# Performance work log

Hardware: AMD Instinct MI355X
Metric: run time of the kernel (lower is better)

## Reference

```python
import jax, jax.numpy as jnp
from jax import lax
import numpy as np

NB_CODE = 16384
DIM = 128
SCALES = [(1, 1), (2, 2), (4, 4), (8, 8), (16, 16)]
PHI_IDX = [0, 1, 1, 2, 3]  # PhiPartiallyShared: argmin(|ticks - si/(SN-1)|), K=4, SN=5
RESI = 0.5  # abs(quant_resi)
BETA = 0.25


def _cubic(x, a=-0.75):
    # PyTorch bicubic kernel (cubic convolution, a=-0.75)
    ax = np.abs(x)
    return np.where(ax <= 1.0, (a + 2.0) * ax ** 3 - (a + 3.0) * ax ** 2 + 1.0,
                    np.where(ax < 2.0, a * ax ** 3 - 5.0 * a * ax ** 2 + 8.0 * a * ax - 4.0 * a, 0.0))


def bicubic_mat(n_in, n_out):
    # 1D interpolation matrix matching torch F.interpolate(mode='bicubic', align_corners=False)
    W = np.zeros((n_out, n_in), dtype=np.float32)
    scale = n_in / n_out
    for i in range(n_out):
        x = (i + 0.5) * scale - 0.5
        x0 = int(np.floor(x))
        t = x - x0
        for k in range(4):
            idx = min(max(x0 - 1 + k, 0), n_in - 1)  # border clamp
            W[i, idx] += _cubic(t + 1.0 - k)
    return jnp.asarray(W)


def phi_apply(h, w, b):
    y = lax.conv_general_dilated(h, w, (1, 1), 'SAME',
                                 dimension_numbers=('NCHW', 'OIHW', 'NCHW'))
    y = y + b[None, :, None, None]
    return h * (1.0 - RESI) + y * RESI


def setup_inputs() -> dict:
    key = jax.random.key(0)
    k1, k2, k3, k4 = jax.random.split(key, 4)
    B, C, J, L = 16, DIM, 16, 16
    f_bcjl = jax.random.normal(k1, (B, C, J, L), dtype=jnp.float32)
    emb = jax.random.normal(k2, (NB_CODE, C), dtype=jnp.float32) * 0.02
    # 4 partially-shared Phi convs (3x3, C->C)
    phi_w = jax.random.normal(k3, (4, C, C, 3, 3), dtype=jnp.float32) * (1.0 / np.sqrt(C * 9))
    phi_b = jax.random.normal(k4, (4, C), dtype=jnp.float32) * 0.01
    return {'f_bcjl': f_bcjl, 'emb': emb, 'phi_w': phi_w, 'phi_b': phi_b}


def reference(f_bcjl, emb, phi_w, phi_b):
    B, C, J, L = f_bcjl.shape
    SN = len(SCALES)
    f_ng = lax.stop_gradient(f_bcjl)
    f_rest = f_ng
    f_hat = jnp.zeros_like(f_ng)
    loss = jnp.float32(0.0)
    e_sq = jnp.sum(emb * emb, axis=1)  # [K]
    idx_all = []
    for si, (sn, tn) in enumerate(SCALES):
        if si != SN - 1:
            # 'area' downsample == integer-factor average pooling here
            r = f_rest.reshape(B, C, sn, J // sn, tn, L // tn).mean(axis=(3, 5))
        else:
            r = f_rest
        rNC = r.transpose(0, 2, 3, 1).reshape(-1, C)  # [N, C]
        d = jnp.sum(rNC * rNC, axis=1, keepdims=True) + e_sq - 2.0 * (rNC @ emb.T)
        idx = jnp.argmin(d, axis=1)  # [N]
        idx_all.append(idx)
        h = emb[idx].reshape(B, sn, tn, C).transpose(0, 3, 1, 2)  # [B,C,sn,tn]
        if si != SN - 1:
            Wj = bicubic_mat(sn, J)
            Wl = bicubic_mat(tn, L)
            h = jnp.einsum('js,bcst,lt->bcjl', Wj, h, Wl)
        k = PHI_IDX[si]
        h = phi_apply(h, phi_w[k], phi_b[k])
        f_hat = f_hat + h
        f_rest = f_rest - h
        loss = loss + BETA * jnp.mean((lax.stop_gradient(f_hat) - f_bcjl) ** 2) \
                    + jnp.mean((f_hat - f_ng) ** 2)
    loss = loss / SN
    idx_cat = jnp.concatenate(idx_all)
    counts = jnp.zeros((NB_CODE,), jnp.float32).at[idx_cat].add(1.0)
    p = counts / idx_cat.shape[0]
    perplexity = jnp.exp(-jnp.sum(p * jnp.log(p + 1e-10)))
    # straight-through estimator
    f_hat_out = lax.stop_gradient(f_hat) - f_ng + f_bcjl
    return (f_hat_out, loss, perplexity)
```

## Files before the change

kernel.cpp:

```cpp
#include <hip/hip_runtime.h>
#include <hip/hip_bf16.h>
#include <math.h>

#define BATCH 16
#define CDIM  128
#define NCODE 16384
#define ELEMS 524288
#define NTOT  5456
#define WEXT_TOT 589824
#define LOSS_COEF 4.76837158203125e-7f

typedef __attribute__((ext_vector_type(8))) short short8;
typedef __attribute__((ext_vector_type(4))) float float4v;
typedef unsigned short ushortT;
typedef unsigned long long u64;
typedef unsigned int u32;

__device__ __forceinline__ ushortT f2bf(float x) {
    __hip_bfloat16 h = __float2bfloat16(x);
    return *reinterpret_cast<ushortT*>(&h);
}
__device__ __forceinline__ float bf2f(ushortT b) {
    __hip_bfloat16 h = *reinterpret_cast<__hip_bfloat16*>(&b);
    return __bfloat162float(h);
}
__device__ __forceinline__ u32 ford(float v) {
    u32 b = __float_as_uint(v);
    return b ^ ((u32)((int)b >> 31) | 0x80000000u);
}

__device__ double cubic_d(double x) {
    const double a = -0.75;
    double ax = fabs(x);
    if (ax <= 1.0) return (a + 2.0) * ax * ax * ax - (a + 3.0) * ax * ax + 1.0;
    if (ax < 2.0)  return a * ax * ax * ax - 5.0 * a * ax * ax + 8.0 * a * ax - 4.0 * a;
    return 0.0;
}

__global__ __launch_bounds__(256)
void k_prologue(const float* __restrict__ f, const float* __restrict__ emb,
                const float* __restrict__ phi_w,
                float* __restrict__ f_rest, float* __restrict__ f_hat,
                float* __restrict__ esq, ushortT* __restrict__ embext,
                ushortT* __restrict__ wext, float* __restrict__ wmat,
                float* __restrict__ lossA) {
    const int t = threadIdx.x;
    const int id = blockIdx.x * 256 + t;

    if (id < ELEMS) {
        f_rest[id] = f[id];
        f_hat[id] = 0.f;
        int row = id >> 5, c4 = id & 31;
        float4 v = reinterpret_cast<const float4*>(emb + (size_t)row * CDIM)[c4];
        float xs[4] = {v.x, v.y, v.z, v.w};
        ushortT hi[4], lo[4];
        float ss = 0.f;
        #pragma unroll
        for (int i = 0; i < 4; ++i) {
            hi[i] = f2bf(xs[i]);
            lo[i] = f2bf(xs[i] - bf2f(hi[i]));
            ss += xs[i] * xs[i];
        }
        ushortT* base = embext + (size_t)row * 256;
        *reinterpret_cast<ushort4*>(base + c4 * 4)       = make_ushort4(hi[0], hi[1], hi[2], hi[3]);
        *reinterpret_cast<ushort4*>(base + 128 + c4 * 4) = make_ushort4(lo[0], lo[1], lo[2], lo[3]);
        #pragma unroll
        for (int off = 16; off; off >>= 1) ss += __shfl_down(ss, off);
        if ((t & 31) == 0) esq[row] = ss;
    }
    if (id < WEXT_TOT) {
        int k4 = id / 147456, rem = id % 147456;
        int co = rem / 1152, kk = rem % 1152;
        int off = kk >> 7, ci = kk & 127;
        float v = 0.5f * phi_w[(((size_t)(k4 * 128 + co)) * 128 + ci) * 9 + off];
        if (ci == co && off == 4) v += 0.5f;
        wext[id] = f2bf(v);
    }
    if (blockIdx.x == 0 && t < 64) {
        int sIdx = t >> 4;
        int S = 1 << sIdx;
        int j = t & 15;
        const int offs[4] = {0, 16, 48, 112};
        double row[8];
        for (int s = 0; s < 8; ++s) row[s] = 0.0;
        double scale = (double)S / 16.0;
        double x = (j + 0.5) * scale - 0.5;
        double x0 = floor(x);
        double tt = x - x0;
        for (int k = 0; k < 4; ++k) {
            int idx = (int)x0 - 1 + k;
            idx = idx < 0 ? 0 : (idx > S - 1 ? S - 1 : idx);
            row[idx] += cubic_d(tt + 1.0 - k);
        }
        for (int s = 0; s < S; ++s) wmat[offs[sIdx] + j * S + s] = (float)row[s];
    }
    if (id == 0) lossA[0] = 0.f;
}

__global__ __launch_bounds__(256)
void k_packext(const float* __restrict__ fr, ushortT* __restrict__ re,
               u64* __restrict__ packed, int N, int padN, int S, int lgS) {
    int id = blockIdx.x * 256 + threadIdx.x;
    if (id < N) packed[id] = ~0ull;
    if (id >= padN * 32) return;
    int row = id >> 5, c4 = id & 31;
    ushortT hi[4], lo[4];
    if (row < N) {
        int mask = S - 1;
        int tt = row & mask, ssi = (row >> lgS) & mask, b = row >> (2 * lgS);
        int bs = 16 >> lgS;
        float inv = 1.f / (float)(bs * bs);
        #pragma unroll
        for (int u = 0; u < 4; ++u) {
            int c = c4 * 4 + u;
            const float* base = fr + (size_t)(b * 128 + c) * 256 + (ssi * bs) * 16 + tt * bs;
            float acc = 0.f;
            for (int jj = 0; jj < bs; ++jj)
                for (int ll = 0; ll < bs; ++ll)
                    acc += base[jj * 16 + ll];
            float x = acc * inv;
            hi[u] = f2bf(x);
            lo[u] = f2bf(x - bf2f(hi[u]));
        }
    } else {
        #pragma unroll
        for (int u = 0; u < 4; ++u) { hi[u] = 0; lo[u] = 0; }
    }
    ushortT* base = re + (size_t)row * 256;
    *reinterpret_cast<ushort4*>(base + c4 * 4)       = make_ushort4(hi[0], hi[1], hi[2], hi[3]);
    *reinterpret_cast<ushort4*>(base + 128 + c4 * 4) = make_ushort4(lo[0], lo[1], lo[2], lo[3]);
}

__global__ __launch_bounds__(256)
void k_packext_wave(const float* __restrict__ fr, ushortT* __restrict__ re,
                    u64* __restrict__ packed, int N, int padN, int S, int lgS) {
    int gid = blockIdx.x * 256 + threadIdx.x;
    int wid = gid >> 6, lane = threadIdx.x & 63;
    if (wid >= padN * 128) return;
    int row = wid >> 7, c = wid & 127;
    float x = 0.f;
    if (row < N) {
        int mask = S - 1;
        int tt = row & mask, ssi = (row >> lgS) & mask, b = row >> (2 * lgS);
        int lgbs = 4 - lgS, bs = 1 << lgbs, cnt = bs * bs;
        const float* base = fr + (size_t)(b * 128 + c) * 256 + (ssi * bs) * 16 + tt * bs;
        float acc = 0.f;
        for (int e = lane; e < cnt; e += 64)
            acc += base[(e >> lgbs) * 16 + (e & (bs - 1))];
        #pragma unroll
        for (int off = 32; off; off >>= 1) acc += __shfl_down(acc, off);
        x = acc / (float)cnt;
    }
    if (lane == 0) {
        ushortT h = f2bf(x);
        re[(size_t)row * 256 + c] = h;
        re[(size_t)row * 256 + 128 + c] = f2bf(x - bf2f(h));
        if (c == 0 && row < N) packed[row] = ~0ull;
    }
}

__global__ __launch_bounds__(256)
void k_argmin_mfma(const ushortT* __restrict__ rext, const ushortT* __restrict__ embext,
                   const float* __restrict__ esq, int N, int kPerSplit,
                   u64* __restrict__ packed) {
    __shared__ ushortT Btile[2][64 * 32 * 8];
    const int t = threadIdx.x;
    const int w = t >> 6;
    const int lane = t & 63;
    const int ln = lane & 15;
    const int q  = lane >> 4;
    const int k0beg = blockIdx.y * kPerSplit;
    const int rowW = blockIdx.x * 128 + w * 32;

    short8 a[2][8];
    {
        const ushortT* r0 = rext + (size_t)(rowW + ln) * 256 + q * 8;
        const ushortT* r1 = rext + (size_t)(rowW + 16 + ln) * 256 + q * 8;
        #pragma unroll
        for (int sb = 0; sb < 8; ++sb) {
            a[0][sb] = *reinterpret_cast<const short8*>(r0 + sb * 32);
            a[1][sb] = *reinterpret_cast<const short8*>(r1 + sb * 32);
        }
    }

    float minv[2][4];
    int   mini[2][4];
    #pragma unroll
    for (int tt = 0; tt < 2; ++tt)
        #pragma unroll
        for (int rg = 0; rg < 4; ++rg) { minv[tt][rg] = 3.4e38f; mini[tt][rg] = 0; }

    const int tiles = kPerSplit >> 6;

    #pragma unroll
    for (int i = 0; i < 8; ++i) {
        int F = (i * 4 + w) * 64 + lane;
        int n = F >> 5, cs = F & 31;
        int cp = (cs & ~7) | ((cs & 7) ^ (n & 7));
        const ushortT* src = embext + (size_t)(k0beg + n) * 256 + cp * 8;
        __builtin_amdgcn_global_load_lds(
            (const __attribute__((address_space(1))) unsigned int*)src,
            (__attribute__((address_space(3))) unsigned int*)&Btile[0][(size_t)((i * 4 + w) * 64) * 8],
            16, 0, 0);
    }

    for (int it = 0; it < tiles; ++it) {
        __syncthreads();
        if (it + 1 < tiles) {
            int k1 = k0beg + (it + 1) * 64;
            int bu = (it + 1) & 1;
            #pragma unroll
            for (int i = 0; i < 8; ++i) {
                int F = (i * 4 + w) * 64 + lane;
                int n = F >> 5, cs = F & 31;
                int cp = (cs & ~7) | ((cs & 7) ^ (n & 7));
                const ushortT* src = embext + (size_t)(k1 + n) * 256 + cp * 8;
                __builtin_amdgcn_global_load_lds(
                    (const __attribute__((address_space(1))) unsigned int*)src,
                    (__attribute__((address_space(3))) unsigned int*)&Btile[bu][(size_t)((i * 4 + w) * 64) * 8],
                    16, 0, 0);
            }
        }
        const ushortT* Bt = Btile[it & 1];
        const int k0 = k0beg + it * 64;

        #pragma unroll
        for (int sub = 0; sub < 4; ++sub) {
            int n = sub * 16 + ln;
            short8 bfr[8];
            #pragma unroll
            for (int sb = 0; sb < 8; ++sb) {
                int cp = q + 4 * sb;
                int cs = (cp & ~7) | ((cp & 7) ^ (n & 7));
                bfr[sb] = *reinterpret_cast<const short8*>(&Bt[(size_t)(n * 32 + cs) * 8]);
            }
            float4v acc0 = {0.f, 0.f, 0.f, 0.f};
            float4v acc1 = {0.f, 0.f, 0.f, 0.f};
            #pragma unroll
            for (int s = 0; s < 12; ++s) {
                int as = s < 8 ? s : s - 8;
                int bs = s < 4 ? s : s - 4;
                acc0 = __builtin_amdgcn_mfma_f32_16x16x32_bf16(a[0][as], bfr[bs], acc0, 0, 0, 0);
                acc1 = __builtin_amdgcn_mfma_f32_16x16x32_bf16(a[1][as], bfr[bs], acc1, 0, 0, 0);
            }
            int kc = k0 + sub * 16 + ln;
            float es = esq[kc];
            #pragma unroll
            for (int rg = 0; rg < 4; ++rg) {
                float sc0 = fmaf(-2.f, acc0[rg], es);
                if (sc0 < minv[0][rg]) { minv[0][rg] = sc0; mini[0][rg] = kc; }
                float sc1 = fmaf(-2.f, acc1[rg], es);
                if (sc1 < minv[1][rg]) { minv[1][rg] = sc1; mini[1][rg] = kc; }
            }
        }
    }

    #pragma unroll
    for (int tt = 0; tt < 2; ++tt)
        #pragma unroll
        for (int rg = 0; rg < 4; ++rg) {
            float v = minv[tt][rg]; int ix = mini[tt][rg];
            #pragma unroll
            for (int off = 1; off < 16; off <<= 1) {
                float ov = __shfl_xor(v, off);
                int   oi = __shfl_xor(ix, off);
                if (ov < v || (ov == v && oi < ix)) { v = ov; ix = oi; }
            }
            if (ln == 0) {
                int row = rowW + tt * 16 + q * 4 + rg;
                if (row < N) {
                    u64 p = ((u64)ford(v) << 32) | (u32)ix;
                    atomicMin(&packed[row], p);
                }
            }
        }
}

__global__ __launch_bounds__(256)
void k_upconv(const float* __restrict__ emb, const u64* __restrict__ packed,
              const float* __restrict__ wm, int S, int lastScale,
              const ushortT* __restrict__ wext, const float* __restrict__ bias,
              const float* __restrict__ f_in, float* __restrict__ f_hat,
              float* __restrict__ f_rest, float* __restrict__ loss_acc) {
    __shared__ __align__(16) ushortT Htile[3 * 16 * 128];
    __shared__ float wsum[4];
    const int t = threadIdx.x;
    const int b = blockIdx.x >> 4;
    const int j = blockIdx.x & 15;

    {
        const int l = t >> 4, c8 = t & 15;
        const int phys = (c8 & 8) | ((c8 & 7) ^ (l & 7));
        #pragma unroll
        for (int r = 0; r < 3; ++r) {
            int jin = j - 1 + r;
            float acc[8] = {0.f, 0.f, 0.f, 0.f, 0.f, 0.f, 0.f, 0.f};
            if (jin >= 0 && jin < 16) {
                if (lastScale) {
                    int idx = (int)(u32)(packed[(b * 16 + jin) * 16 + l] & 0xFFFFFFFFull);
                    const float* er = emb + (size_t)idx * CDIM + c8 * 8;
                    float4 e0 = *reinterpret_cast<const float4*>(er);
                    float4 e1 = *reinterpret_cast<const float4*>(er + 4);
                    acc[0] = e0.x; acc[1] = e0.y; acc[2] = e0.z; acc[3] = e0.w;
                    acc[4] = e1.x; acc[5] = e1.y; acc[6] = e1.z; acc[7] = e1.w;
                } else {
                    for (int s = 0; s < S; ++s) {
                        float wjv = wm[jin * S + s];
                        for (int tt2 = 0; tt2 < S; ++tt2) {
                            float wv = wjv * wm[l * S + tt2];
                            int idx = (int)(u32)(packed[(b * S + s) * S + tt2] & 0xFFFFFFFFull);
                            const float* er = emb + (size_t)idx * CDIM + c8 * 8;
                            float4 e0 = *reinterpret_cast<const float4*>(er);
                            float4 e1 = *reinterpret_cast<const float4*>(er + 4);
                            acc[0] += wv * e0.x; acc[1] += wv * e0.y;
                            acc[2] += wv * e0.z; acc[3] += wv * e0.w;
                            acc[4] += wv * e1.x; acc[5] += wv * e1.y;
                            acc[6] += wv * e1.z; acc[7] += wv * e1.w;
                        }
                    }
                }
            }
            short8 o;
            #pragma unroll
            for (int i = 0; i < 8; ++i) o[i] = (short)f2bf(acc[i]);
            *reinterpret_cast<short8*>(&Htile[((size_t)(r * 16 + l) * 16 + phys) * 8]) = o;
        }
    }
    __syncthreads();

    const int w = t >> 6, lane = t & 63;
    const int ln = lane & 15, q = lane >> 4;
    const int co0 = w * 32;
    const ushortT* wA = wext + (size_t)(co0 + ln) * 1152;
    float4v acc2[2] = {{0.f, 0.f, 0.f, 0.f}, {0.f, 0.f, 0.f, 0.f}};
    const short8 zz = {0, 0, 0, 0, 0, 0, 0, 0};

    #pragma unroll 3
    for (int off = 0; off < 9; ++off) {
        const int dj = off / 3, dl = off % 3;
        int cIn = ln + dl - 1;
        int cCl = cIn < 0 ? 0 : (cIn > 15 ? 15 : cIn);
        bool oob = (cIn != cCl);
        int rb = (dj * 16 + cCl) * 128;
        #pragma unroll
        for (int g = 0; g < 4; ++g) {
            int csl = g * 4 + q;
            int phys = (csl & 8) | ((csl & 7) ^ (cCl & 7));
            short8 av = *reinterpret_cast<const short8*>(&Htile[rb + phys * 8]);
            if (oob) av = zz;
            const ushortT* wr = wA + (off * 4 + g) * 32 + q * 8;
            short8 b0 = *reinterpret_cast<const short8*>(wr);
            short8 b1 = *reinterpret_cast<const short8*>(wr + 16 * 1152);
            acc2[0] = __builtin_amdgcn_mfma_f32_16x16x32_bf16(av, b0, acc2[0], 0, 0, 0);
            acc2[1] = __builtin_amdgcn_mfma_f32_16x16x32_bf16(av, b1, acc2[1], 0, 0, 0);
        }
    }

    float s = 0.f;
    #pragma unroll
    for (int sn = 0; sn < 2; ++sn) {
        int co = co0 + sn * 16 + ln;
        float bsv = 0.5f * bias[co];
        size_t gi = ((size_t)(b * 128 + co) * 16 + j) * 16 + q * 4;
        float4 fh = *reinterpret_cast<const float4*>(&f_hat[gi]);
        float4 fr = *reinterpret_cast<const float4*>(&f_rest[gi]);
        float4 fv = *reinterpret_cast<const float4*>(&f_in[gi]);
        float o0 = acc2[sn][0] + bsv, o1 = acc2[sn][1] + bsv;
        float o2 = acc2[sn][2] + bsv, o3 = acc2[sn][3] + bsv;
        fh.x += o0; fh.y += o1; fh.z += o2; fh.w += o3;
        fr.x -= o0; fr.y -= o1; fr.z -= o2; fr.w -= o3;
        *reinterpret_cast<float4*>(&f_hat[gi]) = fh;
        *reinterpret_cast<float4*>(&f_rest[gi]) = fr;
        float d0 = fh.x - fv.x, d1 = fh.y - fv.y;
        float d2 = fh.z - fv.z, d3 = fh.w - fv.w;
        s += d0 * d0 + d1 * d1 + d2 * d2 + d3 * d3;
    }
    #pragma unroll
    for (int off = 32; off; off >>= 1) s += __shfl_down(s, off);
    if (lane == 0) wsum[w] = s;
    __syncthreads();
    if (t == 0)
        atomicAdd(loss_acc, (wsum[0] + wsum[1] + wsum[2] + wsum[3]) * LOSS_COEF);
}

__global__ __launch_bounds__(256)
void k_final(const u64* __restrict__ packed, const float* __restrict__ loss_acc,
             float* __restrict__ out) {
    __shared__ u32 cnt2[NCODE / 2];
    __shared__ float ws4[4];
    int t = threadIdx.x;
    for (int i = t; i < NCODE / 2; i += 256) cnt2[i] = 0;
    __syncthreads();
    for (int i = t; i < NTOT; i += 256) {
        int idx = (int)(u32)(packed[i] & 0xFFFFFFFFull);
        atomicAdd(&cnt2[idx >> 1], (idx & 1) ? 65536u : 1u);
    }
    __syncthreads();
    float s = 0.f;
    for (int k = t; k < NCODE; k += 256) {
        u32 c = cnt2[k >> 1];
        c = (k & 1) ? (c >> 16) : (c & 0xFFFFu);
        float p = (float)c * (1.0f / (float)NTOT);
        s += p * logf(p + 1e-10f);
    }
    #pragma unroll
    for (int off = 32; off; off >>= 1) s += __shfl_down(s, off);
    if ((t & 63) == 0) ws4[t >> 6] = s;
    __syncthreads();
    if (t == 0) {
        out[ELEMS]     = loss_acc[0];
        out[ELEMS + 1] = expf(-(ws4[0] + ws4[1] + ws4[2] + ws4[3]));
    }
}

extern "C" void kernel_launch(void* const* d_in, const int* in_sizes, int n_in,
                              void* d_out, int out_size, void* d_ws, size_t ws_size,
                              hipStream_t stream) {
    const float* f     = (const float*)d_in[0];
    const float* emb   = (const float*)d_in[1];
    const float* phi_w = (const float*)d_in[2];
    const float* phi_b = (const float*)d_in[3];
    float* out = (float*)d_out;

    float* wsf = (float*)d_ws;
    float*   f_rest = wsf;
    float*   esq    = wsf + 524288;
    float*   wmat   = wsf + 540672;
    float*   lossA  = wsf + 540928;
    u64*     packed = (u64*)(wsf + 540992);
    ushortT* embext = (ushortT*)(wsf + 557376);
    ushortT* rext   = (ushortT*)(wsf + 2654528);
    ushortT* wext   = (ushortT*)(wsf + 3178816);

    k_prologue<<<2304, 256, 0, stream>>>(f, emb, phi_w, f_rest, out, esq,
                                         embext, wext, wmat, lossA);

    const int Ss[5]     = {1, 2, 4, 8, 16};
    const int lgSs[5]   = {0, 1, 2, 3, 4};
    const int phiIdx[5] = {0, 1, 1, 2, 3};
    const int ksplit[5] = {256, 256, 128, 64, 16};
    const int wmOff[5]  = {0, 16, 48, 112, 0};
    const int pOff[5]   = {0, 16, 80, 336, 1360};

    for (int si = 0; si < 5; ++si) {
        int S = Ss[si], lgS = lgSs[si];
        int N = 16 * S * S;
        int padN = (N + 127) & ~127;
        u64* pk = packed + pOff[si];

        if (S <= 2)
            k_packext_wave<<<padN * 128 / 4, 256, 0, stream>>>(f_rest, rext, pk, N, padN, S, lgS);
        else
            k_packext<<<padN * 32 / 256, 256, 0, stream>>>(f_rest, rext, pk, N, padN, S, lgS);

        int KS = ksplit[si];
        k_argmin_mfma<<<dim3(padN / 128, KS), 256, 0, stream>>>(rext, embext, esq,
                                                                N, NCODE / KS, pk);

        int k = phiIdx[si];
        k_upconv<<<256, 256, 0, stream>>>(emb, pk, wmat + wmOff[si], S, si == 4 ? 1 : 0,
                                          wext + (size_t)k * 147456,
                                          phi_b + (size_t)k * 128, f, out, f_rest, lossA);
    }

    k_final<<<1, 256, 0, stream>>>(packed, lossA, out);
}
```

Before: 358.4 us.

## Fuse residual pooling into upconv epilogue and widen argmin row tiles

Removes the separate pack kernels and the f_rest buffer. The residual is now recomputed as f - f_hat, and the next scale's pooled bf16 hi/lo rows are produced in the upconv epilogue. For coarse scales each block reduces them through a shared-memory grid; the scale-0 mean is computed in the prologue. The argmin kernel now covers 64 rows per wave (4 MFMA tiles) with launch bounds of 2 blocks, and k-split counts are retuned. Upconv blocks cover several rows and cache the gathered codebook vectors in LDS. This cuts launches and global traffic at the cost of more registers and shared memory, and fewer blocks at coarse scales.

```diff
diff --git a/kernel.cpp b/kernel.cpp
--- a/kernel.cpp
+++ b/kernel.cpp
@@ -39,16 +39,18 @@
 
 __global__ __launch_bounds__(256)
 void k_prologue(const float* __restrict__ f, const float* __restrict__ emb,
-                const float* __restrict__ phi_w,
-                float* __restrict__ f_rest, float* __restrict__ f_hat,
+                const float* __restrict__ phi_w, float* __restrict__ f_hat,
                 float* __restrict__ esq, ushortT* __restrict__ embext,
                 ushortT* __restrict__ wext, float* __restrict__ wmat,
-                float* __restrict__ lossA) {
+                float* __restrict__ lossA, ushortT* __restrict__ rext,
+                u64* __restrict__ packed) {
+    __shared__ float red[4];
     const int t = threadIdx.x;
-    const int id = blockIdx.x * 256 + t;
-
-    if (id < ELEMS) {
-        f_rest[id] = f[id];
+    const int bid = blockIdx.x;
+    const int id = bid * 256 + t;
+
+    if (bid < 2048) {
+        float fv = f[id];
         f_hat[id] = 0.f;
         int row = id >> 5, c4 = id & 31;
         float4 v = reinterpret_cast<const float4*>(emb + (size_t)row * CDIM)[c4];
@@ -67,6 +69,23 @@
         #pragma unroll
         for (int off = 16; off; off >>= 1) ss += __shfl_down(ss, off);
         if ((t & 31) == 0) esq[row] = ss;
+
+        float s = fv;
+        #pragma unroll
+        for (int off = 32; off; off >>= 1) s += __shfl_down(s, off);
+        if ((t & 63) == 0) red[t >> 6] = s;
+        __syncthreads();
+        if (t == 0) {
+            float m = (red[0] + red[1] + red[2] + red[3]) * (1.f / 256.f);
+            int b = bid >> 7, c = bid & 127;
+            ushortT h = f2bf(m);
+            rext[b * 256 + c] = h;
+            rext[b * 256 + 128 + c] = f2bf(m - bf2f(h));
+        }
+    } else {
+        int idz = (bid - 2048) * 256 + t;
+        if (idz < 30720)
+            reinterpret_cast<u32*>(rext + 16 * 256)[idz] = 0;
     }
     if (id < WEXT_TOT) {
         int k4 = id / 147456, rem = id % 147456;
@@ -76,7 +95,7 @@
         if (ci == co && off == 4) v += 0.5f;
         wext[id] = f2bf(v);
     }
-    if (blockIdx.x == 0 && t < 64) {
+    if (bid == 0 && t < 64) {
         int sIdx = t >> 4;
         int S = 1 << sIdx;
         int j = t & 15;
@@ -95,71 +114,10 @@
         for (int s = 0; s < S; ++s) wmat[offs[sIdx] + j * S + s] = (float)row[s];
     }
     if (id == 0) lossA[0] = 0.f;
-}
-
-__global__ __launch_bounds__(256)
-void k_packext(const float* __restrict__ fr, ushortT* __restrict__ re,
-               u64* __restrict__ packed, int N, int padN, int S, int lgS) {
-    int id = blockIdx.x * 256 + threadIdx.x;
-    if (id < N) packed[id] = ~0ull;
-    if (id >= padN * 32) return;
-    int row = id >> 5, c4 = id & 31;
-    ushortT hi[4], lo[4];
-    if (row < N) {
-        int mask = S - 1;
-        int tt = row & mask, ssi = (row >> lgS) & mask, b = row >> (2 * lgS);
-        int bs = 16 >> lgS;
-        float inv = 1.f / (float)(bs * bs);
-        #pragma unroll
-        for (int u = 0; u < 4; ++u) {
-            int c = c4 * 4 + u;
-            const float* base = fr + (size_t)(b * 128 + c) * 256 + (ssi * bs) * 16 + tt * bs;
-            float acc = 0.f;
-            for (int jj = 0; jj < bs; ++jj)
-                for (int ll = 0; ll < bs; ++ll)
-                    acc += base[jj * 16 + ll];
-            float x = acc * inv;
-            hi[u] = f2bf(x);
-            lo[u] = f2bf(x - bf2f(hi[u]));
-        }
-    } else {
-        #pragma unroll
-        for (int u = 0; u < 4; ++u) { hi[u] = 0; lo[u] = 0; }
-    }
-    ushortT* base = re + (size_t)row * 256;
-    *reinterpret_cast<ushort4*>(base + c4 * 4)       = make_ushort4(hi[0], hi[1], hi[2], hi[3]);
-    *reinterpret_cast<ushort4*>(base + 128 + c4 * 4) = make_ushort4(lo[0], lo[1], lo[2], lo[3]);
-}
-
-__global__ __launch_bounds__(256)
-void k_packext_wave(const float* __restrict__ fr, ushortT* __restrict__ re,
-                    u64* __restrict__ packed, int N, int padN, int S, int lgS) {
-    int gid = blockIdx.x * 256 + threadIdx.x;
-    int wid = gid >> 6, lane = threadIdx.x & 63;
-    if (wid >= padN * 128) return;
-    int row = wid >> 7, c = wid & 127;
-    float x = 0.f;
-    if (row < N) {
-        int mask = S - 1;
-        int tt = row & mask, ssi = (row >> lgS) & mask, b = row >> (2 * lgS);
-        int lgbs = 4 - lgS, bs = 1 << lgbs, cnt = bs * bs;
-        const float* base = fr + (size_t)(b * 128 + c) * 256 + (ssi * bs) * 16 + tt * bs;
-        float acc = 0.f;
-        for (int e = lane; e < cnt; e += 64)
-            acc += base[(e >> lgbs) * 16 + (e & (bs - 1))];
-        #pragma unroll
-        for (int off = 32; off; off >>= 1) acc += __shfl_down(acc, off);
-        x = acc / (float)cnt;
-    }
-    if (lane == 0) {
-        ushortT h = f2bf(x);
-        re[(size_t)row * 256 + c] = h;
-        re[(size_t)row * 256 + 128 + c] = f2bf(x - bf2f(h));
-        if (c == 0 && row < N) packed[row] = ~0ull;
-    }
-}
-
-__global__ __launch_bounds__(256)
+    if (id < 8192) packed[id] = ~0ull;
+}
+
+__global__ __launch_bounds__(256, 2)
 void k_argmin_mfma(const ushortT* __restrict__ rext, const ushortT* __restrict__ embext,
                    const float* __restrict__ esq, int N, int kPerSplit,
                    u64* __restrict__ packed) {
@@ -170,25 +128,23 @@
     const int ln = lane & 15;
     const int q  = lane >> 4;
     const int k0beg = blockIdx.y * kPerSplit;
-    const int rowW = blockIdx.x * 128 + w * 32;
-
-    short8 a[2][8];
-    {
-        const ushortT* r0 = rext + (size_t)(rowW + ln) * 256 + q * 8;
-        const ushortT* r1 = rext + (size_t)(rowW + 16 + ln) * 256 + q * 8;
-        #pragma unroll
-        for (int sb = 0; sb < 8; ++sb) {
-            a[0][sb] = *reinterpret_cast<const short8*>(r0 + sb * 32);
-            a[1][sb] = *reinterpret_cast<const short8*>(r1 + sb * 32);
-        }
-    }
-
-    float minv[2][4];
-    int   mini[2][4];
-    #pragma unroll
-    for (int tt = 0; tt < 2; ++tt)
-        #pragma unroll
-        for (int rg = 0; rg < 4; ++rg) { minv[tt][rg] = 3.4e38f; mini[tt][rg] = 0; }
+    const int rowW = blockIdx.x * 256 + w * 64;
+
+    short8 a[4][8];
+    #pragma unroll
+    for (int ti = 0; ti < 4; ++ti) {
+        const ushortT* r0 = rext + (size_t)(rowW + ti * 16 + ln) * 256 + q * 8;
+        #pragma unroll
+        for (int sb = 0; sb < 8; ++sb)
+            a[ti][sb] = *reinterpret_cast<const short8*>(r0 + sb * 32);
+    }
+
+    float minv[4][4];
+    int   mini[4][4];
+    #pragma unroll
+    for (int ti = 0; ti < 4; ++ti)
+        #pragma unroll
+        for (int rg = 0; rg < 4; ++rg) { minv[ti][rg] = 3.4e38f; mini[ti][rg] = 0; }
 
     const int tiles = kPerSplit >> 6;
 
@@ -234,32 +190,34 @@
                 int cs = (cp & ~7) | ((cp & 7) ^ (n & 7));
                 bfr[sb] = *reinterpret_cast<const short8*>(&Bt[(size_t)(n * 32 + cs) * 8]);
             }
-            float4v acc0 = {0.f, 0.f, 0.f, 0.f};
-            float4v acc1 = {0.f, 0.f, 0.f, 0.f};
+            float4v acc[4];
+            #pragma unroll
+            for (int ti = 0; ti < 4; ++ti) acc[ti] = (float4v){0.f, 0.f, 0.f, 0.f};
             #pragma unroll
             for (int s = 0; s < 12; ++s) {
                 int as = s < 8 ? s : s - 8;
                 int bs = s < 4 ? s : s - 4;
-                acc0 = __builtin_amdgcn_mfma_f32_16x16x32_bf16(a[0][as], bfr[bs], acc0, 0, 0, 0);
-                acc1 = __builtin_amdgcn_mfma_f32_16x16x32_bf16(a[1][as], bfr[bs], acc1, 0, 0, 0);
+                #pragma unroll
+                for (int ti = 0; ti < 4; ++ti)
+                    acc[ti] = __builtin_amdgcn_mfma_f32_16x16x32_bf16(a[ti][as], bfr[bs], acc[ti], 0, 0, 0);
             }
             int kc = k0 + sub * 16 + ln;
             float es = esq[kc];
             #pragma unroll
-            for (int rg = 0; rg < 4; ++rg) {
-                float sc0 = fmaf(-2.f, acc0[rg], es);
-                if (sc0 < minv[0][rg]) { minv[0][rg] = sc0; mini[0][rg] = kc; }
-                float sc1 = fmaf(-2.f, acc1[rg], es);
-                if (sc1 < minv[1][rg]) { minv[1][rg] = sc1; mini[1][rg] = kc; }
-            }
-        }
-    }
-
-    #pragma unroll
-    for (int tt = 0; tt < 2; ++tt)
+            for (int ti = 0; ti < 4; ++ti)
+                #pragma unroll
+                for (int rg = 0; rg < 4; ++rg) {
+                    float sc = fmaf(-2.f, acc[ti][rg], es);
+                    if (sc < minv[ti][rg]) { minv[ti][rg] = sc; mini[ti][rg] = kc; }
+                }
+        }
+    }
+
+    #pragma unroll
+    for (int ti = 0; ti < 4; ++ti)
         #pragma unroll
         for (int rg = 0; rg < 4; ++rg) {
-            float v = minv[tt][rg]; int ix = mini[tt][rg];
+            float v = minv[ti][rg]; int ix = mini[ti][rg];
             #pragma unroll
             for (int off = 1; off < 16; off <<= 1) {
                 float ov = __shfl_xor(v, off);
@@ -267,7 +225,7 @@
                 if (ov < v || (ov == v && oi < ix)) { v = ov; ix = oi; }
             }
             if (ln == 0) {
-                int row = rowW + tt * 16 + q * 4 + rg;
+                int row = rowW + ti * 16 + q * 4 + rg;
                 if (row < N) {
                     u64 p = ((u64)ford(v) << 32) | (u32)ix;
                     atomicMin(&packed[row], p);
@@ -281,19 +239,35 @@
               const float* __restrict__ wm, int S, int lastScale,
               const ushortT* __restrict__ wext, const float* __restrict__ bias,
               const float* __restrict__ f_in, float* __restrict__ f_hat,
-              float* __restrict__ f_rest, float* __restrict__ loss_acc) {
-    __shared__ __align__(16) ushortT Htile[3 * 16 * 128];
+              float* __restrict__ loss_acc,
+              int ROWS, int lgJB, int S2, int lgbs2, ushortT* __restrict__ rext_out) {
+    __shared__ __align__(16) ushortT Htile[10 * 2048];
+    __shared__ float Ecache[8192];
+    __shared__ float pgrid[1024];
     __shared__ float wsum[4];
     const int t = threadIdx.x;
-    const int b = blockIdx.x >> 4;
-    const int j = blockIdx.x & 15;
+    const int jblk = blockIdx.x & ((1 << lgJB) - 1);
+    const int b = blockIdx.x >> lgJB;
+    const int j0 = jblk * ROWS;
+
+    for (int i = t; i < 1024; i += 256) pgrid[i] = 0.f;
+
+    if (!lastScale && S >= 4) {
+        int nC = S * S;
+        float4* E4 = reinterpret_cast<float4*>(Ecache);
+        for (int i = t; i < nC * 32; i += 256) {
+            int code = i >> 5, c4 = i & 31;
+            int idx = (int)(u32)(packed[b * nC + code] & 0xFFFFFFFFull);
+            E4[code * 32 + c4] = reinterpret_cast<const float4*>(emb + (size_t)idx * CDIM)[c4];
+        }
+    }
+    __syncthreads();
 
     {
         const int l = t >> 4, c8 = t & 15;
         const int phys = (c8 & 8) | ((c8 & 7) ^ (l & 7));
-        #pragma unroll
-        for (int r = 0; r < 3; ++r) {
-            int jin = j - 1 + r;
+        for (int r = 0; r < ROWS + 2; ++r) {
+            int jin = j0 - 1 + r;
             float acc[8] = {0.f, 0.f, 0.f, 0.f, 0.f, 0.f, 0.f, 0.f};
             if (jin >= 0 && jin < 16) {
                 if (lastScale) {
@@ -303,12 +277,26 @@
                     float4 e1 = *reinterpret_cast<const float4*>(er + 4);
                     acc[0] = e0.x; acc[1] = e0.y; acc[2] = e0.z; acc[3] = e0.w;
                     acc[4] = e1.x; acc[5] = e1.y; acc[6] = e1.z; acc[7] = e1.w;
+                } else if (S >= 4) {
+                    const float4* E4 = reinterpret_cast<const float4*>(Ecache);
+                    for (int s = 0; s < S; ++s) {
+                        float wjv = wm[jin * S + s];
+                        for (int t2 = 0; t2 < S; ++t2) {
+                            float wv = wjv * wm[l * S + t2];
+                            float4 e0 = E4[(s * S + t2) * 32 + c8 * 2];
+                            float4 e1 = E4[(s * S + t2) * 32 + c8 * 2 + 1];
+                            acc[0] += wv * e0.x; acc[1] += wv * e0.y;
+                            acc[2] += wv * e0.z; acc[3] += wv * e0.w;
+                            acc[4] += wv * e1.x; acc[5] += wv * e1.y;
+                            acc[6] += wv * e1.z; acc[7] += wv * e1.w;
+                        }
+                    }
                 } else {
                     for (int s = 0; s < S; ++s) {
                         float wjv = wm[jin * S + s];
-                        for (int tt2 = 0; tt2 < S; ++tt2) {
-                            float wv = wjv * wm[l * S + tt2];
-                            int idx = (int)(u32)(packed[(b * S + s) * S + tt2] & 0xFFFFFFFFull);
+                        for (int t2 = 0; t2 < S; ++t2) {
+                            float wv = wjv * wm[l * S + t2];
+                            int idx = (int)(u32)(packed[b * S * S + s * S + t2] & 0xFFFFFFFFull);
                             const float* er = emb + (size_t)idx * CDIM + c8 * 8;
                             float4 e0 = *reinterpret_cast<const float4*>(er);
                             float4 e1 = *reinterpret_cast<const float4*>(er + 4);
@@ -332,53 +320,91 @@
     const int ln = lane & 15, q = lane >> 4;
     const int co0 = w * 32;
     const ushortT* wA = wext + (size_t)(co0 + ln) * 1152;
-    float4v acc2[2] = {{0.f, 0.f, 0.f, 0.f}, {0.f, 0.f, 0.f, 0.f}};
     const short8 zz = {0, 0, 0, 0, 0, 0, 0, 0};
-
-    #pragma unroll 3
-    for (int off = 0; off < 9; ++off) {
-        const int dj = off / 3, dl = off % 3;
-        int cIn = ln + dl - 1;
-        int cCl = cIn < 0 ? 0 : (cIn > 15 ? 15 : cIn);
-        bool oob = (cIn != cCl);
-        int rb = (dj * 16 + cCl) * 128;
-        #pragma unroll
-        for (int g = 0; g < 4; ++g) {
-            int csl = g * 4 + q;
-            int phys = (csl & 8) | ((csl & 7) ^ (cCl & 7));
-            short8 av = *reinterpret_cast<const short8*>(&Htile[rb + phys * 8]);
-            if (oob) av = zz;
-            const ushortT* wr = wA + (off * 4 + g) * 32 + q * 8;
-            short8 b0 = *reinterpret_cast<const short8*>(wr);
-            short8 b1 = *reinterpret_cast<const short8*>(wr + 16 * 1152);
-            acc2[0] = __builtin_amdgcn_mfma_f32_16x16x32_bf16(av, b0, acc2[0], 0, 0, 0);
-            acc2[1] = __builtin_amdgcn_mfma_f32_16x16x32_bf16(av, b1, acc2[1], 0, 0, 0);
-        }
-    }
-
     float s = 0.f;
-    #pragma unroll
-    for (int sn = 0; sn < 2; ++sn) {
-        int co = co0 + sn * 16 + ln;
-        float bsv = 0.5f * bias[co];
-        size_t gi = ((size_t)(b * 128 + co) * 16 + j) * 16 + q * 4;
-        float4 fh = *reinterpret_cast<const float4*>(&f_hat[gi]);
-        float4 fr = *reinterpret_cast<const float4*>(&f_rest[gi]);
-        float4 fv = *reinterpret_cast<const float4*>(&f_in[gi]);
-        float o0 = acc2[sn][0] + bsv, o1 = acc2[sn][1] + bsv;
-        float o2 = acc2[sn][2] + bsv, o3 = acc2[sn][3] + bsv;
-        fh.x += o0; fh.y += o1; fh.z += o2; fh.w += o3;
-        fr.x -= o0; fr.y -= o1; fr.z -= o2; fr.w -= o3;
-        *reinterpret_cast<float4*>(&f_hat[gi]) = fh;
-        *reinterpret_cast<float4*>(&f_rest[gi]) = fr;
-        float d0 = fh.x - fv.x, d1 = fh.y - fv.y;
-        float d2 = fh.z - fv.z, d3 = fh.w - fv.w;
-        s += d0 * d0 + d1 * d1 + d2 * d2 + d3 * d3;
-    }
+
+    for (int jt = 0; jt < ROWS; ++jt) {
+        float4v acc2[2] = {{0.f, 0.f, 0.f, 0.f}, {0.f, 0.f, 0.f, 0.f}};
+        #pragma unroll 3
+        for (int off = 0; off < 9; ++off) {
+            const int dj = off / 3, dl = off % 3;
+            int cIn = ln + dl - 1;
+            int cCl = cIn < 0 ? 0 : (cIn > 15 ? 15 : cIn);
+            bool oob = (cIn != cCl);
+            int rb = ((jt + dj) * 16 + cCl) * 128;
+            #pragma unroll
+            for (int g = 0; g < 4; ++g) {
+                int csl = g * 4 + q;
+                int phys = (csl & 8) | ((csl & 7) ^ (cCl & 7));
+                short8 av = *reinterpret_cast<const short8*>(&Htile[rb + phys * 8]);
+                if (oob) av = zz;
+                const ushortT* wr = wA + (off * 4 + g) * 32 + q * 8;
+                short8 b0 = *reinterpret_cast<const short8*>(wr);
+                short8 b1 = *reinterpret_cast<const short8*>(wr + 16 * 1152);
+                acc2[0] = __builtin_amdgcn_mfma_f32_16x16x32_bf16(av, b0, acc2[0], 0, 0, 0);
+                acc2[1] = __builtin_amdgcn_mfma_f32_16x16x32_bf16(av, b1, acc2[1], 0, 0, 0);
+            }
+        }
+        int j = j0 + jt;
+        #pragma unroll
+        for (int sn = 0; sn < 2; ++sn) {
+            int co = co0 + sn * 16 + ln;
+            float bsv = 0.5f * bias[co];
+            size_t gi = ((size_t)(b * 128 + co) * 16 + j) * 16 + q * 4;
+            float4 fh = *reinterpret_cast<const float4*>(&f_hat[gi]);
+            float4 fv = *reinterpret_cast<const float4*>(&f_in[gi]);
+            float fr_[4];
+            float oo[4] = {acc2[sn][0] + bsv, acc2[sn][1] + bsv,
+                           acc2[sn][2] + bsv, acc2[sn][3] + bsv};
+            float fhv[4] = {fh.x + oo[0], fh.y + oo[1], fh.z + oo[2], fh.w + oo[3]};
+            float fvv[4] = {fv.x, fv.y, fv.z, fv.w};
+            *reinterpret_cast<float4*>(&f_hat[gi]) =
+                make_float4(fhv[0], fhv[1], fhv[2], fhv[3]);
+            #pragma unroll
+            for (int i = 0; i < 4; ++i) {
+                float d = fhv[i] - fvv[i];
+                s += d * d;
+                fr_[i] = -d;
+            }
+            if (S2 == 16) {
+                #pragma unroll
+                for (int i = 0; i < 4; ++i) {
+                    int row = (b * 16 + j) * 16 + q * 4 + i;
+                    ushortT hiv = f2bf(fr_[i]);
+                    rext_out[(size_t)row * 256 + co] = hiv;
+                    rext_out[(size_t)row * 256 + 128 + co] = f2bf(fr_[i] - bf2f(hiv));
+                }
+            } else if (S2 > 0) {
+                int t0 = (q * 4) >> lgbs2, t1 = (q * 4 + 3) >> lgbs2;
+                float p0 = 0.f, p1 = 0.f;
+                #pragma unroll
+                for (int i = 0; i < 4; ++i) {
+                    if (((q * 4 + i) >> lgbs2) == t0) p0 += fr_[i]; else p1 += fr_[i];
+                }
+                atomicAdd(&pgrid[co * 8 + t0], p0);
+                if (t1 != t0) atomicAdd(&pgrid[co * 8 + t1], p1);
+            }
+        }
+    }
+
     #pragma unroll
     for (int off = 32; off; off >>= 1) s += __shfl_down(s, off);
     if (lane == 0) wsum[w] = s;
     __syncthreads();
+
+    if (S2 > 0 && S2 < 16) {
+        int bs2 = 1 << lgbs2;
+        float inv = 1.f / (float)(bs2 * bs2);
+        int ss = jblk;
+        for (int i = t; i < S2 * 128; i += 256) {
+            int tt = i >> 7, c = i & 127;
+            float v = pgrid[c * 8 + tt] * inv;
+            int row = (b * S2 + ss) * S2 + tt;
+            ushortT hiv = f2bf(v);
+            rext_out[(size_t)row * 256 + c] = hiv;
+            rext_out[(size_t)row * 256 + 128 + c] = f2bf(v - bf2f(hiv));
+        }
+    }
     if (t == 0)
         atomicAdd(loss_acc, (wsum[0] + wsum[1] + wsum[2] + wsum[3]) * LOSS_COEF);
 }
@@ -423,44 +449,43 @@
     float* out = (float*)d_out;
 
     float* wsf = (float*)d_ws;
-    float*   f_rest = wsf;
-    float*   esq    = wsf + 524288;
-    float*   wmat   = wsf + 540672;
-    float*   lossA  = wsf + 540928;
-    u64*     packed = (u64*)(wsf + 540992);
-    ushortT* embext = (ushortT*)(wsf + 557376);
-    ushortT* rext   = (ushortT*)(wsf + 2654528);
-    ushortT* wext   = (ushortT*)(wsf + 3178816);
-
-    k_prologue<<<2304, 256, 0, stream>>>(f, emb, phi_w, f_rest, out, esq,
-                                         embext, wext, wmat, lossA);
+    float*   esq    = wsf;
+    float*   wmat   = wsf + 16384;
+    float*   lossA  = wsf + 16640;
+    u64*     packed = (u64*)(wsf + 16704);
+    ushortT* embext = (ushortT*)(wsf + 33088);
+    ushortT* rext   = (ushortT*)(wsf + 2130240);
+    ushortT* wext   = (ushortT*)(wsf + 2654528);
+
+    k_prologue<<<2304, 256, 0, stream>>>(f, emb, phi_w, out, esq, embext, wext,
+                                         wmat, lossA, rext, packed);
 
     const int Ss[5]     = {1, 2, 4, 8, 16};
-    const int lgSs[5]   = {0, 1, 2, 3, 4};
     const int phiIdx[5] = {0, 1, 1, 2, 3};
-    const int ksplit[5] = {256, 256, 128, 64, 16};
+    const int ksplit[5] = {256, 256, 256, 64, 32};
     const int wmOff[5]  = {0, 16, 48, 112, 0};
     const int pOff[5]   = {0, 16, 80, 336, 1360};
+    const int ROWSa[5]  = {8, 4, 2, 1, 1};
+    const int lgJBa[5]  = {1, 2, 3, 4, 4};
+    const int S2a[5]    = {2, 4, 8, 16, 0};
+    const int lgbs2a[5] = {3, 2, 1, 0, 0};
 
     for (int si = 0; si < 5; ++si) {
-        int S = Ss[si], lgS = lgSs[si];
+        int S = Ss[si];
         int N = 16 * S * S;
-        int padN = (N + 127) & ~127;
+        int padN = N < 256 ? 256 : N;
+        int KS = ksplit[si];
         u64* pk = packed + pOff[si];
 
-        if (S <= 2)
-            k_packext_wave<<<padN * 128 / 4, 256, 0, stream>>>(f_rest, rext, pk, N, padN, S, lgS);
-        else
-            k_packext<<<padN * 32 / 256, 256, 0, stream>>>(f_rest, rext, pk, N, padN, S, lgS);
-
-        int KS = ksplit[si];
-        k_argmin_mfma<<<dim3(padN / 128, KS), 256, 0, stream>>>(rext, embext, esq,
+        k_argmin_mfma<<<dim3(padN / 256, KS), 256, 0, stream>>>(rext, embext, esq,
                                                                 N, NCODE / KS, pk);
 
         int k = phiIdx[si];
-        k_upconv<<<256, 256, 0, stream>>>(emb, pk, wmat + wmOff[si], S, si == 4 ? 1 : 0,
-                                          wext + (size_t)k * 147456,
-                                          phi_b + (size_t)k * 128, f, out, f_rest, lossA);
+        k_upconv<<<16 * (16 / ROWSa[si]), 256, 0, stream>>>(
+            emb, pk, wmat + wmOff[si], S, si == 4 ? 1 : 0,
+            wext + (size_t)k * 147456, phi_b + (size_t)k * 128,
+            f, out, lossA,
+            ROWSa[si], lgJBa[si], S2a[si], lgbs2a[si], rext);
     }
 
     k_final<<<1, 256, 0, stream>>>(packed, lossA, out);
```

New measurement: 456.5 us. +27.4%, slower.
